# Optimization experiments

Measured on AMD Instinct MI355X. Metric: run time of the kernel, lower is better.

## Reference

```python
import jax, jax.numpy as jnp
import numpy as np

B, W, L = 32768, 5, 20            # batch, words per example, max chars per word
WV, CV = 50000, 100               # word vocab, char vocab
CE, OC, K = 32, 30, 3             # char embed dim, conv out channels (=window_size), kernel
WE, HID, TAGS = 50, 100, 36       # word embed dim, fc1 hidden, output tags


def setup_inputs() -> dict:
    key = jax.random.key(0)
    ks = jax.random.split(key, 8)
    inp = jax.random.randint(ks[0], (B, W, 1 + L), 0, 100, dtype=jnp.int32)
    embedding_matrix = jax.random.normal(ks[1], (WV, WE), jnp.float32).at[0].set(0.0)  # padding_idx=0, frozen
    char_emb = jax.random.normal(ks[2], (CV, CE), jnp.float32).at[0].set(0.0)          # padding_idx=0
    conv_w = jax.random.normal(ks[3], (OC, CE, K), jnp.float32) * 0.1
    conv_b = jnp.zeros((OC,), jnp.float32)
    fc1_w = jax.random.normal(ks[4], (HID, (WE + OC) * W), jnp.float32) * 0.05
    fc1_b = jnp.zeros((HID,), jnp.float32)
    out_w = jax.random.normal(ks[5], (TAGS, HID), jnp.float32) * 0.1
    out_b = jnp.zeros((TAGS,), jnp.float32)
    return dict(input=inp, embedding_matrix=embedding_matrix, char_emb=char_emb,
                conv_w=conv_w, conv_b=conv_b, fc1_w=fc1_w, fc1_b=fc1_b,
                out_w=out_w, out_b=out_b)


def reference(input, embedding_matrix, char_emb, conv_w, conv_b, fc1_w, fc1_b, out_w, out_b):
    b = input.shape[0]
    word_ids = input[:, :, 0]                 # [B, W]
    char_ids = input[:, :, 1:]                # [B, W, L]
    we = embedding_matrix[word_ids]           # [B, W, 50]
    ce = char_emb[char_ids]                   # [B, W, L, CE]
    # conv1d over char axis, batched over all B*W words at once
    x = ce.reshape(b * W, L, CE).transpose(0, 2, 1)        # [B*W, CE, L]
    conv = jax.lax.conv_general_dilated(
        x, conv_w, window_strides=(1,), padding='VALID',
        dimension_numbers=('NCH', 'OIH', 'NCH')) + conv_b[None, :, None]  # [B*W, OC, L-2]
    pooled = conv.max(axis=2).reshape(b, W, OC)            # max pool over time
    feats = jnp.concatenate([we, pooled], axis=-1).reshape(b, -1)  # [B, (50+OC)*W]
    h = jnp.tanh(feats @ fc1_w.T + fc1_b)     # dropout is a no-op at inference
    return h @ out_w.T + out_b                # [B, 36]
```

## Files before the change

### kernel.cpp

```cpp
#include <hip/hip_runtime.h>

#define B_TOT 32768
#define OC 30
#define HID 100
#define TAGS 36

#define WS_TH  0
#define WS_FC1 6000
#define WS_OUT 32624

typedef __attribute__((ext_vector_type(8))) _Float16 half8;
typedef __attribute__((ext_vector_type(2))) _Float16 h2v;
typedef __attribute__((ext_vector_type(4))) float f32x4;

struct __attribute__((packed, aligned(4))) U4A { uint4 v; };

__device__ inline half8 ash8(uint4 u) {
    union { uint4 a; half8 b; } v; v.a = u; return v.b;
}
__device__ inline unsigned int h2u(h2v h) {
    union { h2v a; unsigned int b; } v; v.a = h; return v.b;
}
__device__ inline h2v u2h(unsigned int u) {
    union { unsigned int a; h2v b; } v; v.a = u; return v.b;
}
__device__ inline unsigned int pk_f16(float a, float b) {
    h2v h; h.x = (_Float16)a; h.y = (_Float16)b; return h2u(h);
}
__device__ inline float fast_tanh(float x) {
    float ax = __builtin_fabsf(x);
    float e  = __expf(2.0f * ax);
    float r  = 1.0f - 2.0f * __builtin_amdgcn_rcpf(e + 1.0f);
    return __builtin_copysignf(r, x);
}

__global__ void prep(const float* __restrict__ conv_w,
                     const float* __restrict__ char_emb,
                     const float* __restrict__ fc1_w,
                     const float* __restrict__ out_w,
                     unsigned int* __restrict__ ws) {
    int idx = blockIdx.x * 256 + threadIdx.x;
    if (idx < 6000) {
        int d  = idx & 3;
        int t  = idx >> 2;
        int c  = t % 100;
        int kg = t / 100;
        int g  = kg % 5, k = kg / 5;
        int rd = g * 4 + d;
        float v[2];
        #pragma unroll
        for (int e = 0; e < 2; ++e) {
            int oc = rd * 2 + e;
            float s = 0.f;
            if (oc < OC) {
                for (int ce = 0; ce < 32; ++ce)
                    s += char_emb[c * 32 + ce] * conv_w[(oc * 32 + ce) * 3 + k];
            }
            v[e] = s;
        }
        ws[WS_TH + idx] = pk_f16(v[0], v[1]);
    } else if (idx < 6000 + 23296) {
        int t = idx - 6000;
        int dw = t & 3, lane = (t >> 2) & 63, chunk = t >> 8;
        int ks = chunk / 7, nt = chunk % 7;
        int j = nt * 16 + (lane & 15);
        int k = ks * 32 + (lane >> 4) * 8 + dw * 2;
        float a = (j < HID && k     < 400) ? fc1_w[j * 400 + k]     : 0.f;
        float b = (j < HID && k + 1 < 400) ? fc1_w[j * 400 + k + 1] : 0.f;
        ws[WS_FC1 + ks * 2048 + (nt * 64 + lane) * 4 + dw] = pk_f16(a, b);
    } else if (idx < 29296 + 3072) {
        int t = idx - 29296;
        int dw = t & 3, lane = (t >> 2) & 63, chunk = t >> 8;
        int ks = chunk / 3, nt = chunk % 3;
        int j = nt * 16 + (lane & 15);
        int k = ks * 32 + (lane >> 4) * 8 + dw * 2;
        float a = (j < TAGS && k     < HID) ? out_w[j * 100 + k]     : 0.f;
        float b = (j < TAGS && k + 1 < HID) ? out_w[j * 100 + k + 1] : 0.f;
        ws[WS_OUT + t] = pk_f16(a, b);
    }
}

__global__ __launch_bounds__(256, 2)
void fused(const int*   __restrict__ input,
           const float* __restrict__ emb,
           const float* __restrict__ conv_b,
           const float* __restrict__ fc1_b,
           const float* __restrict__ out_b,
           const unsigned int* __restrict__ ws,
           float*       __restrict__ out)
{
    __shared__ __align__(16) unsigned int Ths[6000];
    __shared__ __align__(16) unsigned int FL[64 * 212];

    const int tid  = threadIdx.x;
    const int wv   = tid >> 6;
    const int lane = tid & 63;
    const int ln15 = lane & 15;
    const int quad = lane >> 4;
    const int gi0  = blockIdx.x * 64 + wv * 16;
    unsigned int* Fw = &FL[wv * (16 * 212)];

    const uint4* srcB = (const uint4*)(ws + WS_FC1);
    const int se = wv * 128 + lane;

    {
        const uint4* src = (const uint4*)(ws + WS_TH);
        uint4* dst = (uint4*)Ths;
        for (int idx = tid; idx < 1500; idx += 256) dst[idx] = src[idx];
    }
    uint4 p0 = srcB[se], p1 = srcB[se + 64];
    __syncthreads();

    #pragma unroll
    for (int r = 0; r < 2; ++r) {
        int idx = lane + r * 64;
        Fw[(idx >> 3) * 212 + 200 + (idx & 7)] = 0;
    }

    {
        int wid[32];
        #pragma unroll
        for (int j = 0; j < 32; ++j) {
            int idx = lane + j * 64;
            if (idx < 2000) {
                int w = (idx / 25) % 5;
                int i = idx / 125;
                wid[j] = input[(gi0 + i) * 105 + w * 21];
            }
        }
        #pragma unroll
        for (int j = 0; j < 32; ++j) {
            int idx = lane + j * 64;
            if (idx < 2000) {
                int ph = idx % 25;
                int w  = (idx / 25) % 5;
                int i  = idx / 125;
                float2 e = *(const float2*)&emb[wid[j] * 50 + ph * 2];
                Fw[i * 212 + w * 40 + ph] = pk_f16(e.x, e.y);
            }
        }
    }

    {
        const int q4  = lane & 3;
        const int oc0 = q4 * 8;
        h2v bias[4];
        #pragma unroll
        for (int d = 0; d < 4; ++d) {
            int a = oc0 + 2 * d, b = a + 1;
            bias[d].x = (_Float16)(a < OC ? conv_b[a] : 0.f);
            bias[d].y = (_Float16)(b < OC ? conv_b[b] : 0.f);
        }
        const unsigned int* T0 = &Ths[q4 * 400];
        const unsigned int* T1 = &Ths[q4 * 400 + 2000];
        const unsigned int* T2 = &Ths[q4 * 400 + 4000];

        const int tk = lane >> 2;
        uint4 cvA0, cvA1, cvA2, cvA3, cvA4;
        {
            const U4A* q = (const U4A*)&input[(gi0 + tk / 5) * 105 + (tk % 5) * 21 + 1];
            cvA0 = q[0].v; cvA1 = q[1].v; cvA2 = q[2].v; cvA3 = q[3].v; cvA4 = q[4].v;
        }
        #pragma unroll
        for (int it = 0; it < 5; ++it) {
            int task = tk + it * 16;
            int i = task / 5, w = task % 5;
            uint4 cvB0, cvB1, cvB2, cvB3, cvB4;
            if (it < 4) {
                int tn = tk + (it + 1) * 16;
                const U4A* q = (const U4A*)&input[(gi0 + tn / 5) * 105 + (tn % 5) * 21 + 1];
                cvB0 = q[0].v; cvB1 = q[1].v; cvB2 = q[2].v; cvB3 = q[3].v; cvB4 = q[4].v;
            }
            int c[20];
            c[0]=cvA0.x; c[1]=cvA0.y; c[2]=cvA0.z; c[3]=cvA0.w;
            c[4]=cvA1.x; c[5]=cvA1.y; c[6]=cvA1.z; c[7]=cvA1.w;
            c[8]=cvA2.x; c[9]=cvA2.y; c[10]=cvA2.z; c[11]=cvA2.w;
            c[12]=cvA3.x; c[13]=cvA3.y; c[14]=cvA3.z; c[15]=cvA3.w;
            c[16]=cvA4.x; c[17]=cvA4.y; c[18]=cvA4.z; c[19]=cvA4.w;
            h2v m[4];
            #pragma unroll
            for (int d = 0; d < 4; ++d) { m[d].x = (_Float16)(-30000.f); m[d].y = (_Float16)(-30000.f); }
            #pragma unroll
            for (int p = 0; p < 18; ++p) {
                uint4 ra = *(const uint4*)&T0[c[p    ] * 4];
                uint4 rb = *(const uint4*)&T1[c[p + 1] * 4];
                uint4 rc = *(const uint4*)&T2[c[p + 2] * 4];
                unsigned int* pa = (unsigned int*)&ra;
                unsigned int* pb = (unsigned int*)&rb;
                unsigned int* pc = (unsigned int*)&rc;
                #pragma unroll
                for (int d = 0; d < 4; ++d) {
                    h2v s = u2h(pa[d]) + u2h(pb[d]) + u2h(pc[d]);
                    m[d] = __builtin_elementwise_max(m[d], s);
                }
            }
            int base = i * 212 + w * 40 + 25 + q4 * 4;
            Fw[base]     = h2u(m[0] + bias[0]);
            Fw[base + 1] = h2u(m[1] + bias[1]);
            Fw[base + 2] = h2u(m[2] + bias[2]);
            if (q4 < 3) Fw[base + 3] = h2u(m[3] + bias[3]);
            cvA0 = cvB0; cvA1 = cvB1; cvA2 = cvB2; cvA3 = cvB3; cvA4 = cvB4;
        }
    }

    uint4 af[13];
    {
        const unsigned int* arow = &Fw[ln15 * 212 + quad * 4];
        #pragma unroll
        for (int ks = 0; ks < 13; ++ks) af[ks] = *(const uint4*)(arow + ks * 16);
    }

    f32x4 acc[7];
    #pragma unroll
    for (int t = 0; t < 7; ++t) acc[t] = f32x4{0, 0, 0, 0};

    uint4* Bb = (uint4*)Ths;
    __syncthreads();
    Bb[se] = p0; Bb[se + 64] = p1;
    __syncthreads();

    #pragma unroll
    for (int ks = 0; ks < 13; ++ks) {
        uint4 n0, n1;
        if (ks < 12) {
            n0 = srcB[(ks + 1) * 512 + se];
            n1 = srcB[(ks + 1) * 512 + se + 64];
        }
        const uint4* bp = Bb + (ks & 1) * 512;
        half8 a = ash8(af[ks]);
        #pragma unroll
        for (int t = 0; t < 7; ++t)
            acc[t] = __builtin_amdgcn_mfma_f32_16x16x32_f16(a, ash8(bp[t * 64 + lane]), acc[t], 0, 0, 0);
        if (ks < 12) {
            uint4* np = Bb + ((ks + 1) & 1) * 512;
            np[se] = n0; np[se + 64] = n1;
        }
        __syncthreads();
    }

    const uint4* srcO = (const uint4*)(ws + WS_OUT);
    uint4 o0 = srcO[wv * 192 + lane];
    uint4 o1 = srcO[wv * 192 + 64 + lane];
    uint4 o2 = srcO[wv * 192 + 128 + lane];

    unsigned int* Hw = Fw;
    {
        for (int t2 = lane; t2 < 224; t2 += 64) {
            int i = t2 / 14, d = t2 % 14;
            Hw[i * 68 + 50 + d] = 0;
        }
        unsigned short* Hs = (unsigned short*)Hw;
        #pragma unroll
        for (int t = 0; t < 7; ++t) {
            int j = t * 16 + ln15;
            if (j < HID) {
                float bj = fc1_b[j];
                #pragma unroll
                for (int r = 0; r < 4; ++r) {
                    int it = quad * 4 + r;
                    float hv = fast_tanh(acc[t][r] + bj);
                    _Float16 h = (_Float16)hv;
                    Hs[it * 136 + j] = *reinterpret_cast<unsigned short*>(&h);
                }
            }
        }
    }

    Bb[wv * 192 + lane]       = o0;
    Bb[wv * 192 + 64 + lane]  = o1;
    Bb[wv * 192 + 128 + lane] = o2;
    __syncthreads();

    {
        f32x4 oacc[3];
        #pragma unroll
        for (int t = 0; t < 3; ++t) oacc[t] = f32x4{0, 0, 0, 0};
        const int aoff = ln15 * 68 + quad * 4;
        #pragma unroll
        for (int ks = 0; ks < 4; ++ks) {
            half8 a = ash8(*(const uint4*)&Hw[aoff + ks * 16]);
            #pragma unroll
            for (int t = 0; t < 3; ++t) {
                uint4 bv = Bb[(ks * 3 + t) * 64 + lane];
                oacc[t] = __builtin_amdgcn_mfma_f32_16x16x32_f16(a, ash8(bv), oacc[t], 0, 0, 0);
            }
        }
        #pragma unroll
        for (int t = 0; t < 3; ++t) {
            int o = t * 16 + ln15;
            if (o < TAGS) {
                float bo = out_b[o];
                #pragma unroll
                for (int r = 0; r < 4; ++r) {
                    int it = gi0 + quad * 4 + r;
                    out[it * TAGS + o] = oacc[t][r] + bo;
                }
            }
        }
    }
}

extern "C" void kernel_launch(void* const* d_in, const int* in_sizes, int n_in,
                              void* d_out, int out_size, void* d_ws, size_t ws_size,
                              hipStream_t stream) {
    const int*   input  = (const int*)  d_in[0];
    const float* emb    = (const float*)d_in[1];
    const float* char_e = (const float*)d_in[2];
    const float* conv_w = (const float*)d_in[3];
    const float* conv_b = (const float*)d_in[4];
    const float* fc1_w  = (const float*)d_in[5];
    const float* fc1_b  = (const float*)d_in[6];
    const float* out_w  = (const float*)d_in[7];
    const float* out_b  = (const float*)d_in[8];
    unsigned int* ws = (unsigned int*)d_ws;

    prep<<<127, 256, 0, stream>>>(conv_w, char_e, fc1_w, out_w, ws);
    fused<<<B_TOT / 64, 256, 0, stream>>>(input, emb, conv_b, fc1_b, out_b, ws, (float*)d_out);
}
```

Baseline: 110.1 us.

## Split each 16-row group across two waves with 512-thread blocks

Doubles the threads per block to 512 while keeping 64 batch rows per block. Each wave now does the embedding gather and char-conv for 8 rows, and pairs of waves share the MFMA work for fc1 and the output layer by splitting the N tiles. The goal is more waves in flight and less serial work per wave, which should hide latency better. The cost is an extra block-wide barrier, uneven tile splits (4 vs 3 fc1 tiles, 2 vs 1 output tiles), and possibly tighter register limits from the 512,4 launch bounds.

```diff
diff --git a/kernel.cpp b/kernel.cpp
--- a/kernel.cpp
+++ b/kernel.cpp
@@ -80,7 +80,7 @@
     }
 }
 
-__global__ __launch_bounds__(256, 2)
+__global__ __launch_bounds__(512, 4)
 void fused(const int*   __restrict__ input,
            const float* __restrict__ emb,
            const float* __restrict__ conv_b,
@@ -97,46 +97,46 @@
     const int lane = tid & 63;
     const int ln15 = lane & 15;
     const int quad = lane >> 4;
-    const int gi0  = blockIdx.x * 64 + wv * 16;
-    unsigned int* Fw = &FL[wv * (16 * 212)];
+    const int grp  = wv >> 1;
+    const int h    = wv & 1;
+    const int gi0  = blockIdx.x * 64 + grp * 16;
+    const int ib0  = blockIdx.x * 64 + wv * 8;
+    unsigned int* Fw8 = &FL[wv * 8 * 212];
+    unsigned int* Fg  = &FL[grp * 16 * 212];
 
     const uint4* srcB = (const uint4*)(ws + WS_FC1);
-    const int se = wv * 128 + lane;
 
     {
         const uint4* src = (const uint4*)(ws + WS_TH);
         uint4* dst = (uint4*)Ths;
-        for (int idx = tid; idx < 1500; idx += 256) dst[idx] = src[idx];
-    }
-    uint4 p0 = srcB[se], p1 = srcB[se + 64];
+        for (int idx = tid; idx < 1500; idx += 512) dst[idx] = src[idx];
+    }
+    uint4 p0{};
+    if (tid < 448) p0 = srcB[tid];
     __syncthreads();
 
-    #pragma unroll
-    for (int r = 0; r < 2; ++r) {
-        int idx = lane + r * 64;
-        Fw[(idx >> 3) * 212 + 200 + (idx & 7)] = 0;
-    }
-
-    {
-        int wid[32];
-        #pragma unroll
-        for (int j = 0; j < 32; ++j) {
+    FL[(tid >> 3) * 212 + 200 + (tid & 7)] = 0;
+
+    {
+        int wid[16];
+        #pragma unroll
+        for (int j = 0; j < 16; ++j) {
             int idx = lane + j * 64;
-            if (idx < 2000) {
+            if (idx < 1000) {
                 int w = (idx / 25) % 5;
                 int i = idx / 125;
-                wid[j] = input[(gi0 + i) * 105 + w * 21];
-            }
-        }
-        #pragma unroll
-        for (int j = 0; j < 32; ++j) {
+                wid[j] = input[(ib0 + i) * 105 + w * 21];
+            }
+        }
+        #pragma unroll
+        for (int j = 0; j < 16; ++j) {
             int idx = lane + j * 64;
-            if (idx < 2000) {
+            if (idx < 1000) {
                 int ph = idx % 25;
                 int w  = (idx / 25) % 5;
                 int i  = idx / 125;
                 float2 e = *(const float2*)&emb[wid[j] * 50 + ph * 2];
-                Fw[i * 212 + w * 40 + ph] = pk_f16(e.x, e.y);
+                Fw8[i * 212 + w * 40 + ph] = pk_f16(e.x, e.y);
             }
         }
     }
@@ -156,144 +156,149 @@
         const unsigned int* T2 = &Ths[q4 * 400 + 4000];
 
         const int tk = lane >> 2;
-        uint4 cvA0, cvA1, cvA2, cvA3, cvA4;
+        uint4 cvA0{}, cvA1{}, cvA2{}, cvA3{}, cvA4{};
         {
-            const U4A* q = (const U4A*)&input[(gi0 + tk / 5) * 105 + (tk % 5) * 21 + 1];
+            const U4A* q = (const U4A*)&input[(ib0 + tk / 5) * 105 + (tk % 5) * 21 + 1];
             cvA0 = q[0].v; cvA1 = q[1].v; cvA2 = q[2].v; cvA3 = q[3].v; cvA4 = q[4].v;
         }
         #pragma unroll
-        for (int it = 0; it < 5; ++it) {
+        for (int it = 0; it < 3; ++it) {
             int task = tk + it * 16;
-            int i = task / 5, w = task % 5;
-            uint4 cvB0, cvB1, cvB2, cvB3, cvB4;
-            if (it < 4) {
+            uint4 cvB0{}, cvB1{}, cvB2{}, cvB3{}, cvB4{};
+            if (it < 2) {
                 int tn = tk + (it + 1) * 16;
-                const U4A* q = (const U4A*)&input[(gi0 + tn / 5) * 105 + (tn % 5) * 21 + 1];
-                cvB0 = q[0].v; cvB1 = q[1].v; cvB2 = q[2].v; cvB3 = q[3].v; cvB4 = q[4].v;
-            }
-            int c[20];
-            c[0]=cvA0.x; c[1]=cvA0.y; c[2]=cvA0.z; c[3]=cvA0.w;
-            c[4]=cvA1.x; c[5]=cvA1.y; c[6]=cvA1.z; c[7]=cvA1.w;
-            c[8]=cvA2.x; c[9]=cvA2.y; c[10]=cvA2.z; c[11]=cvA2.w;
-            c[12]=cvA3.x; c[13]=cvA3.y; c[14]=cvA3.z; c[15]=cvA3.w;
-            c[16]=cvA4.x; c[17]=cvA4.y; c[18]=cvA4.z; c[19]=cvA4.w;
-            h2v m[4];
-            #pragma unroll
-            for (int d = 0; d < 4; ++d) { m[d].x = (_Float16)(-30000.f); m[d].y = (_Float16)(-30000.f); }
-            #pragma unroll
-            for (int p = 0; p < 18; ++p) {
-                uint4 ra = *(const uint4*)&T0[c[p    ] * 4];
-                uint4 rb = *(const uint4*)&T1[c[p + 1] * 4];
-                uint4 rc = *(const uint4*)&T2[c[p + 2] * 4];
-                unsigned int* pa = (unsigned int*)&ra;
-                unsigned int* pb = (unsigned int*)&rb;
-                unsigned int* pc = (unsigned int*)&rc;
+                if (tn < 40) {
+                    const U4A* q = (const U4A*)&input[(ib0 + tn / 5) * 105 + (tn % 5) * 21 + 1];
+                    cvB0 = q[0].v; cvB1 = q[1].v; cvB2 = q[2].v; cvB3 = q[3].v; cvB4 = q[4].v;
+                }
+            }
+            if (task < 40) {
+                int i = task / 5, w = task % 5;
+                int c[20];
+                c[0]=cvA0.x; c[1]=cvA0.y; c[2]=cvA0.z; c[3]=cvA0.w;
+                c[4]=cvA1.x; c[5]=cvA1.y; c[6]=cvA1.z; c[7]=cvA1.w;
+                c[8]=cvA2.x; c[9]=cvA2.y; c[10]=cvA2.z; c[11]=cvA2.w;
+                c[12]=cvA3.x; c[13]=cvA3.y; c[14]=cvA3.z; c[15]=cvA3.w;
+                c[16]=cvA4.x; c[17]=cvA4.y; c[18]=cvA4.z; c[19]=cvA4.w;
+                h2v m[4];
                 #pragma unroll
-                for (int d = 0; d < 4; ++d) {
-                    h2v s = u2h(pa[d]) + u2h(pb[d]) + u2h(pc[d]);
-                    m[d] = __builtin_elementwise_max(m[d], s);
+                for (int d = 0; d < 4; ++d) { m[d].x = (_Float16)(-30000.f); m[d].y = (_Float16)(-30000.f); }
+                #pragma unroll
+                for (int p = 0; p < 18; ++p) {
+                    uint4 ra = *(const uint4*)&T0[c[p    ] * 4];
+                    uint4 rb = *(const uint4*)&T1[c[p + 1] * 4];
+                    uint4 rc = *(const uint4*)&T2[c[p + 2] * 4];
+                    unsigned int* pa = (unsigned int*)&ra;
+                    unsigned int* pb = (unsigned int*)&rb;
+                    unsigned int* pc = (unsigned int*)&rc;
+                    #pragma unroll
+                    for (int d = 0; d < 4; ++d) {
+                        h2v s = u2h(pa[d]) + u2h(pb[d]) + u2h(pc[d]);
+                        m[d] = __builtin_elementwise_max(m[d], s);
+                    }
                 }
-            }
-            int base = i * 212 + w * 40 + 25 + q4 * 4;
-            Fw[base]     = h2u(m[0] + bias[0]);
-            Fw[base + 1] = h2u(m[1] + bias[1]);
-            Fw[base + 2] = h2u(m[2] + bias[2]);
-            if (q4 < 3) Fw[base + 3] = h2u(m[3] + bias[3]);
+                int base = i * 212 + w * 40 + 25 + q4 * 4;
+                Fw8[base]     = h2u(m[0] + bias[0]);
+                Fw8[base + 1] = h2u(m[1] + bias[1]);
+                Fw8[base + 2] = h2u(m[2] + bias[2]);
+                if (q4 < 3) Fw8[base + 3] = h2u(m[3] + bias[3]);
+            }
             cvA0 = cvB0; cvA1 = cvB1; cvA2 = cvB2; cvA3 = cvB3; cvA4 = cvB4;
         }
     }
+    __syncthreads();
 
     uint4 af[13];
     {
-        const unsigned int* arow = &Fw[ln15 * 212 + quad * 4];
+        const unsigned int* arow = &Fg[ln15 * 212 + quad * 4];
         #pragma unroll
         for (int ks = 0; ks < 13; ++ks) af[ks] = *(const uint4*)(arow + ks * 16);
     }
 
-    f32x4 acc[7];
+    f32x4 acc[4];
     #pragma unroll
-    for (int t = 0; t < 7; ++t) acc[t] = f32x4{0, 0, 0, 0};
+    for (int t = 0; t < 4; ++t) acc[t] = f32x4{0, 0, 0, 0};
+    const int nt0 = h * 4;
 
     uint4* Bb = (uint4*)Ths;
-    __syncthreads();
-    Bb[se] = p0; Bb[se + 64] = p1;
+    if (tid < 448) Bb[tid] = p0;
     __syncthreads();
 
     #pragma unroll
     for (int ks = 0; ks < 13; ++ks) {
-        uint4 n0, n1;
-        if (ks < 12) {
-            n0 = srcB[(ks + 1) * 512 + se];
-            n1 = srcB[(ks + 1) * 512 + se + 64];
-        }
+        uint4 n0{};
+        if (ks < 12 && tid < 448)
+            n0 = srcB[(ks + 1) * 512 + tid];
         const uint4* bp = Bb + (ks & 1) * 512;
         half8 a = ash8(af[ks]);
         #pragma unroll
-        for (int t = 0; t < 7; ++t)
-            acc[t] = __builtin_amdgcn_mfma_f32_16x16x32_f16(a, ash8(bp[t * 64 + lane]), acc[t], 0, 0, 0);
-        if (ks < 12) {
-            uint4* np = Bb + ((ks + 1) & 1) * 512;
-            np[se] = n0; np[se + 64] = n1;
-        }
+        for (int t = 0; t < 3; ++t)
+            acc[t] = __builtin_amdgcn_mfma_f32_16x16x32_f16(a, ash8(bp[(nt0 + t) * 64 + lane]), acc[t], 0, 0, 0);
+        if (h == 0)
+            acc[3] = __builtin_amdgcn_mfma_f32_16x16x32_f16(a, ash8(bp[3 * 64 + lane]), acc[3], 0, 0, 0);
+        if (ks < 12 && tid < 448)
+            Bb[((ks + 1) & 1) * 512 + tid] = n0;
         __syncthreads();
     }
 
     const uint4* srcO = (const uint4*)(ws + WS_OUT);
-    uint4 o0 = srcO[wv * 192 + lane];
-    uint4 o1 = srcO[wv * 192 + 64 + lane];
-    uint4 o2 = srcO[wv * 192 + 128 + lane];
-
-    unsigned int* Hw = Fw;
-    {
-        for (int t2 = lane; t2 < 224; t2 += 64) {
-            int i = t2 / 14, d = t2 % 14;
-            Hw[i * 68 + 50 + d] = 0;
-        }
-        unsigned short* Hs = (unsigned short*)Hw;
-        #pragma unroll
-        for (int t = 0; t < 7; ++t) {
-            int j = t * 16 + ln15;
+    uint4 og0 = srcO[tid];
+    uint4 og1{};
+    if (tid < 256) og1 = srcO[512 + tid];
+
+    unsigned short* Hs = (unsigned short*)Fg;
+    {
+        for (int t2 = lane + h * 64; t2 < 288; t2 += 128) {
+            int i = t2 / 18, d = t2 % 18;
+            Fg[i * 68 + 50 + d] = 0;
+        }
+        #pragma unroll
+        for (int t = 0; t < 4; ++t) {
+            if (h == 1 && t == 3) break;
+            int j = (nt0 + t) * 16 + ln15;
             if (j < HID) {
                 float bj = fc1_b[j];
                 #pragma unroll
                 for (int r = 0; r < 4; ++r) {
                     int it = quad * 4 + r;
                     float hv = fast_tanh(acc[t][r] + bj);
-                    _Float16 h = (_Float16)hv;
-                    Hs[it * 136 + j] = *reinterpret_cast<unsigned short*>(&h);
+                    _Float16 hh = (_Float16)hv;
+                    Hs[it * 136 + j] = *reinterpret_cast<unsigned short*>(&hh);
                 }
             }
         }
     }
 
-    Bb[wv * 192 + lane]       = o0;
-    Bb[wv * 192 + 64 + lane]  = o1;
-    Bb[wv * 192 + 128 + lane] = o2;
+    Bb[tid] = og0;
+    if (tid < 256) Bb[512 + tid] = og1;
     __syncthreads();
 
     {
-        f32x4 oacc[3];
-        #pragma unroll
-        for (int t = 0; t < 3; ++t) oacc[t] = f32x4{0, 0, 0, 0};
+        f32x4 oacc[2];
+        oacc[0] = f32x4{0, 0, 0, 0};
+        oacc[1] = f32x4{0, 0, 0, 0};
+        const int tb0 = h ? 2 : 0;
+        const int ntt = h ? 1 : 2;
         const int aoff = ln15 * 68 + quad * 4;
         #pragma unroll
         for (int ks = 0; ks < 4; ++ks) {
-            half8 a = ash8(*(const uint4*)&Hw[aoff + ks * 16]);
+            half8 a = ash8(*(const uint4*)&Fg[aoff + ks * 16]);
             #pragma unroll
-            for (int t = 0; t < 3; ++t) {
-                uint4 bv = Bb[(ks * 3 + t) * 64 + lane];
-                oacc[t] = __builtin_amdgcn_mfma_f32_16x16x32_f16(a, ash8(bv), oacc[t], 0, 0, 0);
-            }
-        }
-        #pragma unroll
-        for (int t = 0; t < 3; ++t) {
-            int o = t * 16 + ln15;
-            if (o < TAGS) {
-                float bo = out_b[o];
-                #pragma unroll
-                for (int r = 0; r < 4; ++r) {
-                    int it = gi0 + quad * 4 + r;
-                    out[it * TAGS + o] = oacc[t][r] + bo;
+            for (int t = 0; t < 2; ++t)
+                if (t < ntt)
+                    oacc[t] = __builtin_amdgcn_mfma_f32_16x16x32_f16(a, ash8(Bb[(ks * 3 + tb0 + t) * 64 + lane]), oacc[t], 0, 0, 0);
+        }
+        #pragma unroll
+        for (int t = 0; t < 2; ++t) {
+            if (t < ntt) {
+                int o = (tb0 + t) * 16 + ln15;
+                if (o < TAGS) {
+                    float bo = out_b[o];
+                    #pragma unroll
+                    for (int r = 0; r < 4; ++r) {
+                        int it = gi0 + quad * 4 + r;
+                        out[it * TAGS + o] = oacc[t][r] + bo;
+                    }
                 }
             }
         }
@@ -315,5 +320,5 @@
     unsigned int* ws = (unsigned int*)d_ws;
 
     prep<<<127, 256, 0, stream>>>(conv_w, char_e, fc1_w, out_w, ws);
-    fused<<<B_TOT / 64, 256, 0, stream>>>(input, emb, conv_b, fc1_b, out_b, ws, (float*)d_out);
-}
+    fused<<<B_TOT / 64, 512, 0, stream>>>(input, emb, conv_b, fc1_b, out_b, ws, (float*)d_out);
+}
```

Result: slower. 185.6 us (+68.5%).
